# Performance work log

Measured on AMD Instinct MI355X. Metric: run time of the kernel, lower is better.

The kernel has to match this reference:

```python
import jax, jax.numpy as jnp
import numpy as np

DEPTH_MIN = 0.0
DEPTH_MAX = 1.0
NUM_BINS = 64
LOSS_WEIGHT = 1.0
EPS = 1e-12  # torch F.normalize default eps


def setup_inputs() -> dict:
    key = jax.random.key(0)
    k1, k2, k3 = jax.random.split(key, 3)
    N, C, H, W = 4, 256, 128, 160
    preds_S = jax.random.normal(k1, (N, C, H, W), jnp.float32)
    preds_T = jax.random.normal(k2, (N, C, H, W), jnp.float32)
    depth_gt_resized = jax.random.uniform(k3, (N, 1, H, W), jnp.float32)
    return {"preds_S": preds_S, "preds_T": preds_T, "depth_gt_resized": depth_gt_resized}


def _bin_indices_ud(depth):
    # Uniform discretization (mode='UD'), target=True clamping semantics
    bin_size = (DEPTH_MAX - DEPTH_MIN) / NUM_BINS
    idx = (depth - DEPTH_MIN) / bin_size
    invalid = (idx < 0) | (idx > NUM_BINS) | ~jnp.isfinite(idx)
    idx = jnp.where(invalid, NUM_BINS, idx)
    return idx.astype(jnp.int32)  # truncation toward zero, matches torch int64 cast for >=0 values


def _protos(feats, idx):
    # feats: (P, C) pixel features; idx: (P,) bin ids in [0, NUM_BINS]
    # segment mean per bin, then L2-normalize along channels -> (NUM_BINS, C)
    sums = jax.ops.segment_sum(feats, idx, num_segments=NUM_BINS + 1)
    counts = jax.ops.segment_sum(jnp.ones(idx.shape, feats.dtype), idx, num_segments=NUM_BINS + 1)
    means = sums[:NUM_BINS] / jnp.maximum(counts[:NUM_BINS, None], 1.0)
    norm = jnp.linalg.norm(means, axis=1, keepdims=True)
    return means / jnp.maximum(norm, EPS)


def reference(preds_S, preds_T, depth_gt_resized):
    N, C, H, W = preds_S.shape
    idx = _bin_indices_ud(depth_gt_resized[:, 0]).reshape(-1)  # (N*H*W,)
    # pixels-major layout: (N, H, W, C) -> (P, C)
    fS = preds_S.transpose(0, 2, 3, 1).reshape(-1, C)
    fT = preds_T.transpose(0, 2, 3, 1).reshape(-1, C)
    pS = _protos(fS, idx)  # (bins, C)
    pT = _protos(fT, idx)
    sim_S = pS @ pS.T  # (bins, bins)
    sim_T = pT @ pT.T
    return LOSS_WEIGHT * jnp.mean((sim_S - sim_T) ** 2)
```

## Files before the change

### kernel.cpp

```cpp
#include <hip/hip_runtime.h>

#define NB     64
#define CCH    256
#define HW     20480
#define PXB    1024
#define NPR    (HW/PXB)
#define GRID_MS (2*4*16*NPR)

#define REP_STRIDE (2 * NB * CCH)
#define WS_COUNTS 262144
#define WS_ACC    262404
#define WS_TICKET 262408
#define WS_ZERO   262412
#define WS_PS     131072
#define WS_PT     196608

typedef __attribute__((ext_vector_type(8))) short short8;
typedef __attribute__((ext_vector_type(4))) float f32x4;

#define ROWSTR 1032

__global__ __launch_bounds__(256, 4)
void k_msum(const float* __restrict__ predsS,
            const float* __restrict__ predsT,
            const float* __restrict__ depth,
            float* __restrict__ sums,
            int* __restrict__ counts) {
    int tid = threadIdx.x;
    int blk = blockIdx.x;
    int prange = blk % NPR;
    int group  = blk / NPR;
    int tensor = group >> 6;
    int n  = (group >> 4) & 3;
    int cg = group & 15;
    int px0 = prange * PXB;

    const float* xbase = (tensor ? predsT : predsS)
                       + (size_t)(n * CCH + cg * 16) * HW + px0;
    const float* dbase = depth + n * HW + px0;

    __shared__ short sAll[16][ROWSTR];
    __shared__ unsigned char sBin[PXB];
    __shared__ int lhist[NB + 1];

    int lane = tid & 63, wv = tid >> 6;
    int l15 = lane & 15, q = lane >> 4;

    float dv[4];
    #pragma unroll
    for (int r = 0; r < 4; ++r) dv[r] = dbase[tid + r * 256];

    const float* rbase = xbase + (size_t)(wv * 4) * HW;
    float4 vv[8];
    #pragma unroll
    for (int c = 0; c < 4; ++c)
        vv[c] = *(const float4*)(rbase + c * 256 + lane * 4);
    #pragma unroll
    for (int c = 0; c < 4; ++c)
        vv[4 + c] = *(const float4*)(rbase + HW + c * 256 + lane * 4);

    bool desig = (tensor == 0) && (cg == 0);
    if (desig && tid < NB + 1) lhist[tid] = 0;

    #pragma unroll
    for (int r = 0; r < 4; ++r) {
        float f = dv[r] * 64.0f;
        int b;
        if (!(f >= 0.0f) || f > 64.0f) b = NB;
        else b = (int)f;
        sBin[tid + r * 256] = (unsigned char)b;
    }

    #pragma unroll
    for (int rr = 0; rr < 4; ++rr) {
        int s = (rr & 1) * 4;
        #pragma unroll
        for (int c = 0; c < 4; ++c) {
            unsigned u0 = __float_as_uint(vv[s + c].x), u1 = __float_as_uint(vv[s + c].y);
            unsigned u2 = __float_as_uint(vv[s + c].z), u3 = __float_as_uint(vv[s + c].w);
            uint2 hv;
            hv.x = ((u0 + 0x8000u) >> 16) | ((u1 + 0x8000u) & 0xFFFF0000u);
            hv.y = ((u2 + 0x8000u) >> 16) | ((u3 + 0x8000u) & 0xFFFF0000u);
            *(uint2*)&sAll[wv * 4 + rr][c * 256 + lane * 4] = hv;
        }
        if (rr < 2) {
            #pragma unroll
            for (int c = 0; c < 4; ++c)
                vv[s + c] = *(const float4*)(rbase + (size_t)(rr + 2) * HW + c * 256 + lane * 4);
        }
    }

    f32x4 acc[4];
    #pragma unroll
    for (int mt = 0; mt < 4; ++mt) acc[mt] = (f32x4)0.0f;

    __syncthreads();

    #pragma unroll
    for (int ks = 0; ks < 8; ++ks) {
        int pk = wv * 256 + ks * 32 + q * 8;
        unsigned long long bv = *(const unsigned long long*)&sBin[pk];
        short8 bHi = *(const short8*)&sAll[l15][pk];
        #pragma unroll
        for (int mt = 0; mt < 4; ++mt) {
            int tgt = mt * 16 + l15;
            short8 afr;
            #pragma unroll
            for (int j = 0; j < 8; ++j)
                afr[j] = ((int)((bv >> (8 * j)) & 0xFFull) == tgt) ? (short)0x3F80 : (short)0;
            acc[mt] = __builtin_amdgcn_mfma_f32_16x16x32_bf16(afr, bHi, acc[mt], 0, 0, 0);
        }
    }

    __syncthreads();
    float* red = (float*)&sAll[0][0];
    #pragma unroll
    for (int mt = 0; mt < 4; ++mt)
        #pragma unroll
        for (int r = 0; r < 4; ++r)
            red[wv * 1024 + (mt * 16 + q * 4 + r) * 16 + l15] = acc[mt][r];
    if (desig) {
        for (int i = tid; i < PXB; i += 256) atomicAdd(&lhist[sBin[i]], 1);
    }
    __syncthreads();
    float* dst = sums + (size_t)(blk & 1) * REP_STRIDE
               + (size_t)tensor * NB * CCH + cg * 16;
    #pragma unroll
    for (int k = 0; k < 4; ++k) {
        int e = tid + k * 256;
        float s = red[e] + red[1024 + e] + red[2048 + e] + red[3072 + e];
        atomicAdd(&dst[(e >> 4) * CCH + (e & 15)], s);
    }
    if (desig && tid < NB + 1 && lhist[tid] != 0) atomicAdd(&counts[tid], lhist[tid]);
}

__global__ __launch_bounds__(256) void k_protos(const float* __restrict__ sums,
                                                const int* __restrict__ counts,
                                                float* __restrict__ pS,
                                                float* __restrict__ pT) {
    int b = blockIdx.x, t = threadIdx.x;
    int ci = counts[b];
    float cnt = (float)(ci < 1 ? 1 : ci);
    float mS = (sums[b * CCH + t] + sums[REP_STRIDE + b * CCH + t]) / cnt;
    float mT = (sums[(NB + b) * CCH + t] + sums[REP_STRIDE + (NB + b) * CCH + t]) / cnt;
    float ss = mS * mS, st = mT * mT;
    #pragma unroll
    for (int o = 32; o; o >>= 1) {
        ss += __shfl_xor(ss, o, 64);
        st += __shfl_xor(st, o, 64);
    }
    __shared__ float rs[4], rt[4];
    int w = t >> 6;
    if ((t & 63) == 0) { rs[w] = ss; rt[w] = st; }
    __syncthreads();
    float nS = sqrtf(rs[0] + rs[1] + rs[2] + rs[3]);
    float nT = sqrtf(rt[0] + rt[1] + rt[2] + rt[3]);
    pS[b * CCH + t] = mS / fmaxf(nS, 1e-12f);
    pT[b * CCH + t] = mT / fmaxf(nT, 1e-12f);
}

__global__ __launch_bounds__(256) void k_sim(const float* __restrict__ pS,
                                             const float* __restrict__ pT,
                                             float* __restrict__ acc,
                                             unsigned int* __restrict__ ticket,
                                             float* __restrict__ out) {
    int i = blockIdx.x;
    int t = threadIdx.x;
    int j = t & 63, seg = t >> 6;
    __shared__ float rowS[CCH], rowT[CCH];
    rowS[t] = pS[i * CCH + t];
    rowT[t] = pT[i * CCH + t];
    __syncthreads();
    const float4* Sj = (const float4*)(pS + j * CCH + seg * 64);
    const float4* Tj = (const float4*)(pT + j * CCH + seg * 64);
    const float4* Si = (const float4*)(rowS + seg * 64);
    const float4* Ti = (const float4*)(rowT + seg * 64);
    float dS = 0.0f, dT = 0.0f;
    #pragma unroll
    for (int k = 0; k < 16; ++k) {
        float4 a = Si[k], b = Sj[k];
        dS += a.x * b.x + a.y * b.y + a.z * b.z + a.w * b.w;
        float4 c = Ti[k], d = Tj[k];
        dT += c.x * d.x + c.y * d.y + c.z * d.z + c.w * d.w;
    }
    __shared__ float sS[4][64], sT[4][64];
    sS[seg][j] = dS;
    sT[seg][j] = dT;
    __syncthreads();
    if (t < 64) {
        float fS = sS[0][t] + sS[1][t] + sS[2][t] + sS[3][t];
        float fT = sT[0][t] + sT[1][t] + sT[2][t] + sT[3][t];
        float e = fS - fT;
        e = e * e;
        #pragma unroll
        for (int o = 32; o; o >>= 1) e += __shfl_xor(e, o, 64);
        if (t == 0) {
            atomicAdd(acc, e);
            __threadfence();
            unsigned int r = atomicAdd(ticket, 1u);
            if (r == NB - 1) {
                float tot = atomicAdd(acc, 0.0f);
                out[0] = tot * (1.0f / (float)(NB * NB));
            }
        }
    }
}

extern "C" void kernel_launch(void* const* d_in, const int* in_sizes, int n_in,
                              void* d_out, int out_size, void* d_ws, size_t ws_size,
                              hipStream_t stream) {
    const float* predsS = (const float*)d_in[0];
    const float* predsT = (const float*)d_in[1];
    const float* depth  = (const float*)d_in[2];
    char* ws = (char*)d_ws;
    float* sums = (float*)ws;
    int* counts = (int*)(ws + WS_COUNTS);
    float* acc = (float*)(ws + WS_ACC);
    unsigned int* ticket = (unsigned int*)(ws + WS_TICKET);
    float* pS = (float*)(ws + WS_PS);
    float* pT = (float*)(ws + WS_PT);

    hipMemsetAsync(ws, 0, WS_ZERO, stream);
    k_msum<<<GRID_MS, 256, 0, stream>>>(predsS, predsT, depth, sums, counts);
    k_protos<<<NB, 256, 0, stream>>>(sums, counts, pS, pT);
    k_sim<<<NB, 256, 0, stream>>>(pS, pT, acc, ticket, (float*)d_out);
}
```

Baseline: 199.7 us.

## Load MFMA B-fragments directly from global and fuse proto and sim kernels

The segment-sum kernel now has each lane load its MFMA B-operand pixels directly from global memory and converts them to bf16 in registers. This removes the 32KB LDS staging buffer, raises the occupancy hint to 6, and double-buffers the loads across k-steps. The prototype normalisation and similarity kernels are merged into one kernel, which removes a launch and the pS/pT round trip. In exchange, every block recomputes all 64 norms and the j-side prototypes from the sums, and the direct per-lane loads are less coalesced.

```diff
diff --git a/kernel.cpp b/kernel.cpp
--- a/kernel.cpp
+++ b/kernel.cpp
@@ -12,15 +12,11 @@
 #define WS_ACC    262404
 #define WS_TICKET 262408
 #define WS_ZERO   262412
-#define WS_PS     131072
-#define WS_PT     196608
 
 typedef __attribute__((ext_vector_type(8))) short short8;
 typedef __attribute__((ext_vector_type(4))) float f32x4;
 
-#define ROWSTR 1032
-
-__global__ __launch_bounds__(256, 4)
+__global__ __launch_bounds__(256, 6)
 void k_msum(const float* __restrict__ predsS,
             const float* __restrict__ predsT,
             const float* __restrict__ depth,
@@ -39,9 +35,9 @@
                        + (size_t)(n * CCH + cg * 16) * HW + px0;
     const float* dbase = depth + n * HW + px0;
 
-    __shared__ short sAll[16][ROWSTR];
     __shared__ unsigned char sBin[PXB];
     __shared__ int lhist[NB + 1];
+    __shared__ float red[4096];
 
     int lane = tid & 63, wv = tid >> 6;
     int l15 = lane & 15, q = lane >> 4;
@@ -50,14 +46,13 @@
     #pragma unroll
     for (int r = 0; r < 4; ++r) dv[r] = dbase[tid + r * 256];
 
-    const float* rbase = xbase + (size_t)(wv * 4) * HW;
-    float4 vv[8];
-    #pragma unroll
-    for (int c = 0; c < 4; ++c)
-        vv[c] = *(const float4*)(rbase + c * 256 + lane * 4);
-    #pragma unroll
-    for (int c = 0; c < 4; ++c)
-        vv[4 + c] = *(const float4*)(rbase + HW + c * 256 + lane * 4);
+    const float* fb = xbase + (size_t)l15 * HW + wv * 256 + q * 8;
+    float4 va[4], vb[4];
+    #pragma unroll
+    for (int p = 0; p < 4; ++p) {
+        va[p] = *(const float4*)(fb + p * 32);
+        vb[p] = *(const float4*)(fb + p * 32 + 4);
+    }
 
     bool desig = (tensor == 0) && (cg == 0);
     if (desig && tid < NB + 1) lhist[tid] = 0;
@@ -71,25 +66,6 @@
         sBin[tid + r * 256] = (unsigned char)b;
     }
 
-    #pragma unroll
-    for (int rr = 0; rr < 4; ++rr) {
-        int s = (rr & 1) * 4;
-        #pragma unroll
-        for (int c = 0; c < 4; ++c) {
-            unsigned u0 = __float_as_uint(vv[s + c].x), u1 = __float_as_uint(vv[s + c].y);
-            unsigned u2 = __float_as_uint(vv[s + c].z), u3 = __float_as_uint(vv[s + c].w);
-            uint2 hv;
-            hv.x = ((u0 + 0x8000u) >> 16) | ((u1 + 0x8000u) & 0xFFFF0000u);
-            hv.y = ((u2 + 0x8000u) >> 16) | ((u3 + 0x8000u) & 0xFFFF0000u);
-            *(uint2*)&sAll[wv * 4 + rr][c * 256 + lane * 4] = hv;
-        }
-        if (rr < 2) {
-            #pragma unroll
-            for (int c = 0; c < 4; ++c)
-                vv[s + c] = *(const float4*)(rbase + (size_t)(rr + 2) * HW + c * 256 + lane * 4);
-        }
-    }
-
     f32x4 acc[4];
     #pragma unroll
     for (int mt = 0; mt < 4; ++mt) acc[mt] = (f32x4)0.0f;
@@ -98,9 +74,22 @@
 
     #pragma unroll
     for (int ks = 0; ks < 8; ++ks) {
-        int pk = wv * 256 + ks * 32 + q * 8;
-        unsigned long long bv = *(const unsigned long long*)&sBin[pk];
-        short8 bHi = *(const short8*)&sAll[l15][pk];
+        int pi = ks & 3;
+        unsigned long long bv = *(const unsigned long long*)&sBin[wv * 256 + ks * 32 + q * 8];
+        float4 A = va[pi], B = vb[pi];
+        unsigned u0 = __float_as_uint(A.x), u1 = __float_as_uint(A.y);
+        unsigned u2 = __float_as_uint(A.z), u3 = __float_as_uint(A.w);
+        unsigned u4 = __float_as_uint(B.x), u5 = __float_as_uint(B.y);
+        unsigned u6 = __float_as_uint(B.z), u7 = __float_as_uint(B.w);
+        union { short8 s; unsigned u[4]; } bh;
+        bh.u[0] = ((u0 + 0x8000u) >> 16) | ((u1 + 0x8000u) & 0xFFFF0000u);
+        bh.u[1] = ((u2 + 0x8000u) >> 16) | ((u3 + 0x8000u) & 0xFFFF0000u);
+        bh.u[2] = ((u4 + 0x8000u) >> 16) | ((u5 + 0x8000u) & 0xFFFF0000u);
+        bh.u[3] = ((u6 + 0x8000u) >> 16) | ((u7 + 0x8000u) & 0xFFFF0000u);
+        if (ks < 4) {
+            va[pi] = *(const float4*)(fb + (ks + 4) * 32);
+            vb[pi] = *(const float4*)(fb + (ks + 4) * 32 + 4);
+        }
         #pragma unroll
         for (int mt = 0; mt < 4; ++mt) {
             int tgt = mt * 16 + l15;
@@ -108,12 +97,10 @@
             #pragma unroll
             for (int j = 0; j < 8; ++j)
                 afr[j] = ((int)((bv >> (8 * j)) & 0xFFull) == tgt) ? (short)0x3F80 : (short)0;
-            acc[mt] = __builtin_amdgcn_mfma_f32_16x16x32_bf16(afr, bHi, acc[mt], 0, 0, 0);
-        }
-    }
-
-    __syncthreads();
-    float* red = (float*)&sAll[0][0];
+            acc[mt] = __builtin_amdgcn_mfma_f32_16x16x32_bf16(afr, bh.s, acc[mt], 0, 0, 0);
+        }
+    }
+
     #pragma unroll
     for (int mt = 0; mt < 4; ++mt)
         #pragma unroll
@@ -134,54 +121,70 @@
     if (desig && tid < NB + 1 && lhist[tid] != 0) atomicAdd(&counts[tid], lhist[tid]);
 }
 
-__global__ __launch_bounds__(256) void k_protos(const float* __restrict__ sums,
-                                                const int* __restrict__ counts,
-                                                float* __restrict__ pS,
-                                                float* __restrict__ pT) {
-    int b = blockIdx.x, t = threadIdx.x;
-    int ci = counts[b];
-    float cnt = (float)(ci < 1 ? 1 : ci);
-    float mS = (sums[b * CCH + t] + sums[REP_STRIDE + b * CCH + t]) / cnt;
-    float mT = (sums[(NB + b) * CCH + t] + sums[REP_STRIDE + (NB + b) * CCH + t]) / cnt;
-    float ss = mS * mS, st = mT * mT;
-    #pragma unroll
-    for (int o = 32; o; o >>= 1) {
-        ss += __shfl_xor(ss, o, 64);
-        st += __shfl_xor(st, o, 64);
-    }
-    __shared__ float rs[4], rt[4];
-    int w = t >> 6;
-    if ((t & 63) == 0) { rs[w] = ss; rt[w] = st; }
-    __syncthreads();
-    float nS = sqrtf(rs[0] + rs[1] + rs[2] + rs[3]);
-    float nT = sqrtf(rt[0] + rt[1] + rt[2] + rt[3]);
-    pS[b * CCH + t] = mS / fmaxf(nS, 1e-12f);
-    pT[b * CCH + t] = mT / fmaxf(nT, 1e-12f);
-}
-
-__global__ __launch_bounds__(256) void k_sim(const float* __restrict__ pS,
-                                             const float* __restrict__ pT,
-                                             float* __restrict__ acc,
-                                             unsigned int* __restrict__ ticket,
-                                             float* __restrict__ out) {
-    int i = blockIdx.x;
-    int t = threadIdx.x;
-    int j = t & 63, seg = t >> 6;
+__global__ __launch_bounds__(256) void k_psim(const float* __restrict__ sums,
+                                              const int* __restrict__ counts,
+                                              float* __restrict__ acc,
+                                              unsigned int* __restrict__ ticket,
+                                              float* __restrict__ out) {
+    int i = blockIdx.x, t = threadIdx.x;
+    int lane = t & 63, w = t >> 6;
     __shared__ float rowS[CCH], rowT[CCH];
-    rowS[t] = pS[i * CCH + t];
-    rowT[t] = pT[i * CCH + t];
-    __syncthreads();
-    const float4* Sj = (const float4*)(pS + j * CCH + seg * 64);
-    const float4* Tj = (const float4*)(pT + j * CCH + seg * 64);
+    __shared__ float partS[NB][4], partT[NB][4];
+    __shared__ float nS[NB], nT[NB];
+
+    for (int s = 0; s < NB; ++s) {
+        int ci = counts[s];
+        float cnt = (float)(ci < 1 ? 1 : ci);
+        float mS = (sums[s * CCH + t] + sums[REP_STRIDE + s * CCH + t]) / cnt;
+        float mT = (sums[(NB + s) * CCH + t] + sums[REP_STRIDE + (NB + s) * CCH + t]) / cnt;
+        if (s == i) { rowS[t] = mS; rowT[t] = mT; }
+        float ss = mS * mS, st = mT * mT;
+        #pragma unroll
+        for (int o = 32; o; o >>= 1) {
+            ss += __shfl_xor(ss, o, 64);
+            st += __shfl_xor(st, o, 64);
+        }
+        if (lane == 0) { partS[s][w] = ss; partT[s][w] = st; }
+    }
+    __syncthreads();
+    if (t < NB) {
+        nS[t] = fmaxf(sqrtf(partS[t][0] + partS[t][1] + partS[t][2] + partS[t][3]), 1e-12f);
+        nT[t] = fmaxf(sqrtf(partT[t][0] + partT[t][1] + partT[t][2] + partT[t][3]), 1e-12f);
+    }
+    __syncthreads();
+    rowS[t] = rowS[t] / nS[i];
+    rowT[t] = rowT[t] / nT[i];
+    __syncthreads();
+
+    int j = lane, seg = w;
+    int cj = counts[j];
+    float cntj = (float)(cj < 1 ? 1 : cj);
+    float nSj = nS[j], nTj = nT[j];
+    const float4* aS = (const float4*)(sums + j * CCH + seg * 64);
+    const float4* bS = (const float4*)(sums + REP_STRIDE + j * CCH + seg * 64);
+    const float4* aT = (const float4*)(sums + (NB + j) * CCH + seg * 64);
+    const float4* bT = (const float4*)(sums + REP_STRIDE + (NB + j) * CCH + seg * 64);
     const float4* Si = (const float4*)(rowS + seg * 64);
     const float4* Ti = (const float4*)(rowT + seg * 64);
     float dS = 0.0f, dT = 0.0f;
     #pragma unroll
     for (int k = 0; k < 16; ++k) {
-        float4 a = Si[k], b = Sj[k];
-        dS += a.x * b.x + a.y * b.y + a.z * b.z + a.w * b.w;
-        float4 c = Ti[k], d = Tj[k];
-        dT += c.x * d.x + c.y * d.y + c.z * d.z + c.w * d.w;
+        float4 x = aS[k], y = bS[k];
+        float4 pj;
+        pj.x = ((x.x + y.x) / cntj) / nSj;
+        pj.y = ((x.y + y.y) / cntj) / nSj;
+        pj.z = ((x.z + y.z) / cntj) / nSj;
+        pj.w = ((x.w + y.w) / cntj) / nSj;
+        float4 a = Si[k];
+        dS += a.x * pj.x + a.y * pj.y + a.z * pj.z + a.w * pj.w;
+        float4 u = aT[k], v = bT[k];
+        float4 qj;
+        qj.x = ((u.x + v.x) / cntj) / nTj;
+        qj.y = ((u.y + v.y) / cntj) / nTj;
+        qj.z = ((u.z + v.z) / cntj) / nTj;
+        qj.w = ((u.w + v.w) / cntj) / nTj;
+        float4 c = Ti[k];
+        dT += c.x * qj.x + c.y * qj.y + c.z * qj.z + c.w * qj.w;
     }
     __shared__ float sS[4][64], sT[4][64];
     sS[seg][j] = dS;
@@ -217,11 +220,8 @@
     int* counts = (int*)(ws + WS_COUNTS);
     float* acc = (float*)(ws + WS_ACC);
     unsigned int* ticket = (unsigned int*)(ws + WS_TICKET);
-    float* pS = (float*)(ws + WS_PS);
-    float* pT = (float*)(ws + WS_PT);
 
     hipMemsetAsync(ws, 0, WS_ZERO, stream);
     k_msum<<<GRID_MS, 256, 0, stream>>>(predsS, predsT, depth, sums, counts);
-    k_protos<<<NB, 256, 0, stream>>>(sums, counts, pS, pT);
-    k_sim<<<NB, 256, 0, stream>>>(pS, pT, acc, ticket, (float*)d_out);
+    k_psim<<<NB, 256, 0, stream>>>(sums, counts, acc, ticket, (float*)d_out);
 }
```

Result: slower. 252.7 us (+26.6%).
